# Kernel optimization log

Measured on AMD Instinct MI355X. Metric: run time of the kernel, lower is better.

The kernel has to match this reference:

```python
import jax, jax.numpy as jnp
import numpy as np

L1, L2, B = 512, 512, 2
D1, D2, BN = 256, 256, 256
NEG = jnp.float32(-1e12)


def setup_inputs() -> dict:
    key = jax.random.key(0)
    ks = jax.random.split(key, 8)
    s = 0.05
    return {
        "ctx_1": jax.random.normal(ks[0], (L1, B, D1), jnp.float32),
        "ctx_2": jax.random.normal(ks[1], (L2, B, D2), jnp.float32),
        "ctx_1_mask": jnp.ones((L1, B), jnp.float32),
        "ctx_2_mask": jnp.ones((L2, B), jnp.float32),
        # mlp_hid: Conv2d(D1+D2 -> BN, 1x1) with bias
        "Wh": jax.random.normal(ks[2], (D1 + D2, BN), jnp.float32) * s,
        "bh": jnp.zeros((BN,), jnp.float32),
        # mlp_out: Conv2d(BN -> 1, 1x1), bias=False (mlp_bias default)
        "wo": jax.random.normal(ks[3], (BN,), jnp.float32) * s,
        # project_1_to_2 / project_2_to_1: Linear(D1+D2 -> BN) with bias
        "W12": jax.random.normal(ks[4], (D2 + D1, BN), jnp.float32) * s,
        "b12": jnp.zeros((BN,), jnp.float32),
        "W21": jax.random.normal(ks[5], (D1 + D2, BN), jnp.float32) * s,
        "b21": jnp.zeros((BN,), jnp.float32),
    }


def reference(ctx_1, ctx_2, ctx_1_mask, ctx_2_mask, Wh, bh, wo, W12, b12, W21, b21):
    d1 = ctx_1.shape[-1]
    # 1x1 conv on cat([b_ctx_1, b_ctx_2]) == sum of two independent projections
    Wh1, Wh2 = Wh[:d1], Wh[d1:]
    p1 = jnp.einsum('lbd,dk->blk', ctx_1, Wh1)            # (B, L1, K)
    p2 = jnp.einsum('mbd,dk->bmk', ctx_2, Wh2)            # (B, L2, K)
    hidden = jnp.tanh(p1[:, :, None, :] + p2[:, None, :, :] + bh)  # (B, L1, L2, K)
    affinity = jnp.einsum('blmk,k->blm', hidden, wo)      # (B, L1, L2)
    # masked in both directions
    affinity = affinity + (1.0 - ctx_1_mask.T)[:, :, None] * NEG
    affinity = affinity + (1.0 - ctx_2_mask.T)[:, None, :] * NEG
    # 1 -> 2 direction: softmax over L2
    dist_1_to_2 = jax.nn.softmax(affinity, axis=2)        # (B, L1, L2)
    context_1_to_2 = jnp.einsum('lbd,blm->mbd', ctx_1, dist_1_to_2)  # (L2, B, D1)
    seq_1_to_2 = jnp.tanh(jnp.concatenate([ctx_2, context_1_to_2], axis=-1) @ W12 + b12)
    # 2 -> 1 direction: softmax over L1 (then contracted over L2, as in the torch code)
    dist_2_to_1 = jax.nn.softmax(affinity, axis=1)        # (B, L1, L2)
    context_2_to_1 = jnp.einsum('mbd,blm->lbd', ctx_2, dist_2_to_1)  # (L1, B, D2)
    seq_2_to_1 = jnp.tanh(jnp.concatenate([ctx_1, context_2_to_1], axis=-1) @ W21 + b21)
    return (seq_2_to_1, seq_1_to_2)
```

## Files before the change

### kernel.cpp

```cpp
#include <hip/hip_runtime.h>


#define NEGC (-1e12f)
#define TWO_LOG2E 2.8853900817779268f
#define LOG2E 1.4426950408889634f
#define N2LOG2E (-2.8853900817779268f)

typedef __attribute__((ext_vector_type(8))) short bf16x8;
typedef __attribute__((ext_vector_type(4))) float f32x4;

__device__ __forceinline__ short f2bf(float x)
{
    union { float f; unsigned u; } v; v.f = x;
    unsigned r = (v.u + 0x7FFFu + ((v.u >> 16) & 1u)) >> 16;
    return (short)r;
}

__global__ __launch_bounds__(256) void k_proj(
    const float* __restrict__ ctx1, const float* __restrict__ ctx2,
    const float* __restrict__ Wh, const float* __restrict__ bh,
    const float* __restrict__ W12, const float* __restrict__ b12,
    const float* __restrict__ W21, const float* __restrict__ b21,
    const float* __restrict__ mask1, const float* __restrict__ mask2,
    float* __restrict__ E1, float* __restrict__ E2,
    float* __restrict__ P12, float* __restrict__ U1,
    float* __restrict__ P21, float* __restrict__ U2,
    float* __restrict__ p1, float* __restrict__ p2,
    float* __restrict__ S1, float* __restrict__ S2)
{
    const int t  = threadIdx.x;
    const int g  = blockIdx.z;
    const int r0 = blockIdx.x * 64;
    const int n0 = blockIdx.y * 64;

    const float* A; const float* W; const float* bias; int expm; float* outp;
    switch (g) {
      case 0:  A=ctx1; W=Wh;        bias=bh;   expm=1; outp=E1;  break;
      case 1:  A=ctx2; W=Wh+65536;  bias=0;    expm=1; outp=E2;  break;
      case 2:  A=ctx2; W=W12;       bias=b12;  expm=0; outp=P12; break;
      case 3:  A=ctx1; W=W12+65536; bias=0;    expm=0; outp=U1;  break;
      case 4:  A=ctx1; W=W21;       bias=b21;  expm=0; outp=P21; break;
      default: A=ctx2; W=W21+65536; bias=0;    expm=0; outp=U2;  break;
    }

    if (g == 0 && blockIdx.x == 0 && blockIdx.y == 0) {
        for (int idx = t; idx < 1024; idx += 256) {
            int row = idx >> 1, b = idx & 1;
            p1[b * 512 + row] = __builtin_amdgcn_exp2f(LOG2E * (1.f - mask1[idx]) * NEGC);
            p2[b * 512 + row] = __builtin_amdgcn_exp2f(LOG2E * (1.f - mask2[idx]) * NEGC);
            S1[b * 512 + row] = 0.f;
            S2[b * 512 + row] = 0.f;
        }
    }

    __shared__ __align__(16) short Abf[64 * 136];
    __shared__ __align__(16) short Bbf[64 * 136];

    const int w    = t >> 6;
    const int lane = t & 63;
    const int quad = lane >> 4;
    const int lr   = lane & 15;

    f32x4 acc[4] = {};

    for (int kc = 0; kc < 256; kc += 128) {
        #pragma unroll
        for (int i = 0; i < 8; ++i) {
            int slot = i * 256 + t;
            int r = slot >> 5, kq = (slot & 31) << 2;
            float4 v = *(const float4*)(A + (r0 + r) * 256 + kc + kq);
            short4 s; s.x = f2bf(v.x); s.y = f2bf(v.y); s.z = f2bf(v.z); s.w = f2bf(v.w);
            *(short4*)(Abf + r * 136 + kq) = s;
        }
        #pragma unroll
        for (int i = 0; i < 8; ++i) {
            int slot = i * 256 + t;
            int bk = slot >> 4, bn4 = (slot & 15) << 2;
            float4 v = *(const float4*)(W + (kc + bk) * 256 + n0 + bn4);
            Bbf[(bn4 + 0) * 136 + bk] = f2bf(v.x);
            Bbf[(bn4 + 1) * 136 + bk] = f2bf(v.y);
            Bbf[(bn4 + 2) * 136 + bk] = f2bf(v.z);
            Bbf[(bn4 + 3) * 136 + bk] = f2bf(v.w);
        }
        __syncthreads();
        #pragma unroll
        for (int s = 0; s < 4; ++s) {
            const int kb = s * 32 + quad * 8;
            bf16x8 a = *(const bf16x8*)(Abf + (w * 16 + lr) * 136 + kb);
            #pragma unroll
            for (int nc = 0; nc < 4; ++nc) {
                bf16x8 b = *(const bf16x8*)(Bbf + (nc * 16 + lr) * 136 + kb);
                acc[nc] = __builtin_amdgcn_mfma_f32_16x16x32_bf16(a, b, acc[nc], 0, 0, 0);
            }
        }
        __syncthreads();
    }

    #pragma unroll
    for (int nc = 0; nc < 4; ++nc) {
        const int col = n0 + nc * 16 + lr;
        const float bv = bias ? bias[col] : 0.f;
        #pragma unroll
        for (int reg = 0; reg < 4; ++reg) {
            int row  = r0 + w * 16 + quad * 4 + reg;
            int orow = ((row & 1) << 9) + (row >> 1);
            float v = acc[nc][reg] + bv;
            if (expm) v = __builtin_amdgcn_exp2f(v * TWO_LOG2E);
            outp[orow * 256 + col] = v;
        }
    }
}

#define PAIR(AV, QV, WV, ACC) do {                                    \
    float x0_ = fmaf(AV.x, QV.x, 1.f);                                \
    float x1_ = fmaf(AV.y, QV.y, 1.f);                                \
    float x2_ = fmaf(AV.z, QV.z, 1.f);                                \
    float x3_ = fmaf(AV.w, QV.w, 1.f);                                \
    float r01_ = __builtin_amdgcn_rcpf(x0_ * x1_);                    \
    float r23_ = __builtin_amdgcn_rcpf(x2_ * x3_);                    \
    float z01_ = fmaf(WV.y, x0_, WV.x * x1_);                         \
    float z23_ = fmaf(WV.w, x2_, WV.z * x3_);                         \
    ACC = fmaf(r01_, z01_, ACC);                                      \
    ACC = fmaf(r23_, z23_, ACC);                                      \
} while (0)

__global__ __launch_bounds__(256) void k_aff(
    const float* __restrict__ E1g, const float* __restrict__ E2g,
    const float* __restrict__ wo,
    const float* __restrict__ p1g, const float* __restrict__ p2g,
    float* __restrict__ EN, float* __restrict__ ET,
    float* __restrict__ S1, float* __restrict__ S2)
{
    const int t  = threadIdx.x;
    const int l0 = blockIdx.x * 32, m0 = blockIdx.y * 32, b = blockIdx.z;

    __shared__ __align__(16) float E1s[32 * 132];
    __shared__ __align__(16) float E2s[32 * 132];
    __shared__ __align__(16) float affs[32 * 36];

    const int tl = t >> 4, tm = t & 15;
    float acc[2][2] = {};

    for (int kc = 0; kc < 256; kc += 128) {
        #pragma unroll
        for (int i = 0; i < 4; ++i) {
            int slot = i * 256 + t;
            int r = slot >> 5, kq = (slot & 31) << 2;
            *(float4*)(E1s + r * 132 + kq) =
                *(const float4*)(E1g + (((b << 9) + l0 + r) << 8) + kc + kq);
            *(float4*)(E2s + r * 132 + kq) =
                *(const float4*)(E2g + (((b << 9) + m0 + r) << 8) + kc + kq);
        }
        __syncthreads();
        #pragma unroll 4
        for (int k0 = 0; k0 < 128; k0 += 4) {
            const float4 w  = *(const float4*)(wo + kc + k0);
            const float4 a0 = *(const float4*)(E1s + tl * 132 + k0);
            const float4 a1 = *(const float4*)(E1s + (tl + 16) * 132 + k0);
            const float4 q0 = *(const float4*)(E2s + tm * 132 + k0);
            const float4 q1 = *(const float4*)(E2s + (tm + 16) * 132 + k0);
            PAIR(a0, q0, w, acc[0][0]);
            PAIR(a0, q1, w, acc[0][1]);
            PAIR(a1, q0, w, acc[1][0]);
            PAIR(a1, q1, w, acc[1][1]);
        }
        __syncthreads();
    }

    affs[tl * 36 + tm]             = __builtin_amdgcn_exp2f(acc[0][0] * N2LOG2E);
    affs[tl * 36 + tm + 16]        = __builtin_amdgcn_exp2f(acc[0][1] * N2LOG2E);
    affs[(tl + 16) * 36 + tm]      = __builtin_amdgcn_exp2f(acc[1][0] * N2LOG2E);
    affs[(tl + 16) * 36 + tm + 16] = __builtin_amdgcn_exp2f(acc[1][1] * N2LOG2E);
    __syncthreads();

    const int r  = t >> 3;
    const int c4 = (t & 7) << 2;
    {
        float4 e = *(const float4*)(affs + r * 36 + c4);
        const float p1r = p1g[(b << 9) + l0 + r];
        float4 vn = make_float4(e.x * p1r, e.y * p1r, e.z * p1r, e.w * p1r);
        *(float4*)(EN + (((b << 9) + l0 + r) << 9) + m0 + c4) = vn;
        float4 p2v = *(const float4*)(p2g + (b << 9) + m0 + c4);
        float s = (e.x * p2v.x + e.y * p2v.y) + (e.z * p2v.z + e.w * p2v.w);
        s += __shfl_xor(s, 1, 64);
        s += __shfl_xor(s, 2, 64);
        s += __shfl_xor(s, 4, 64);
        if ((t & 7) == 0) atomicAdd(S1 + (b << 9) + l0 + r, s);
    }
    {
        float4 te;
        te.x = affs[(c4 + 0) * 36 + r];
        te.y = affs[(c4 + 1) * 36 + r];
        te.z = affs[(c4 + 2) * 36 + r];
        te.w = affs[(c4 + 3) * 36 + r];
        const float p2r = p2g[(b << 9) + m0 + r];
        float4 vt = make_float4(te.x * p2r, te.y * p2r, te.z * p2r, te.w * p2r);
        *(float4*)(ET + (((b << 9) + m0 + r) << 9) + l0 + c4) = vt;
        float4 p1v = *(const float4*)(p1g + (b << 9) + l0 + c4);
        float s = (te.x * p1v.x + te.y * p1v.y) + (te.z * p1v.z + te.w * p1v.w);
        s += __shfl_xor(s, 1, 64);
        s += __shfl_xor(s, 2, 64);
        s += __shfl_xor(s, 4, 64);
        if ((t & 7) == 0) atomicAdd(S2 + (b << 9) + m0 + r, s);
    }
}

__global__ __launch_bounds__(256) void k_final(
    const float* __restrict__ EN, const float* __restrict__ ET,
    const float* __restrict__ U1, const float* __restrict__ U2,
    const float* __restrict__ P12, const float* __restrict__ P21,
    const float* __restrict__ S1, const float* __restrict__ S2,
    float* __restrict__ out)
{
    const int t   = threadIdx.x;
    const int r0  = blockIdx.x * 32, n0 = blockIdx.y * 32;
    const int dir = blockIdx.z >> 1, b = blockIdx.z & 1;
    const float* Ag = (dir == 0 ? ET  : EN)  + b * 262144;
    const float* Sg = (dir == 0 ? S1  : S2)  + b * 512;
    const float* Bg = (dir == 0 ? U1  : U2)  + b * 131072;
    const float* Pg = (dir == 0 ? P12 : P21) + b * 131072;
    float* o = out + (dir == 0 ? 262144 : 0);

    __shared__ __align__(16) short Abf[32 * 72];
    __shared__ __align__(16) short Bbf[32 * 72];
    __shared__ __align__(16) float rs[512];

    for (int i = t; i < 512; i += 256)
        rs[i] = __builtin_amdgcn_rcpf(Sg[i]);
    __syncthreads();

    const int w    = t >> 6;
    const int lane = t & 63;
    const int quad = lane >> 4;
    const int lr   = lane & 15;
    const int wr   = (w >> 1) << 4, wc = (w & 1) << 4;
    f32x4 acc = {};

    for (int kc = 0; kc < 512; kc += 64) {
        #pragma unroll
        for (int i = 0; i < 2; ++i) {
            int slot = i * 256 + t;
            int r = slot >> 4, kq = (slot & 15) << 2;
            float4 v = *(const float4*)(Ag + ((r0 + r) << 9) + kc + kq);
            const float* rp = rs + kc + kq;
            short4 s;
            s.x = f2bf(v.x * rp[0]); s.y = f2bf(v.y * rp[1]);
            s.z = f2bf(v.z * rp[2]); s.w = f2bf(v.w * rp[3]);
            *(short4*)(Abf + r * 72 + kq) = s;
        }
        #pragma unroll
        for (int i = 0; i < 2; ++i) {
            int slot = i * 256 + t;
            int bk = slot >> 3, bn4 = (slot & 7) << 2;
            float4 v = *(const float4*)(Bg + ((kc + bk) << 8) + n0 + bn4);
            Bbf[(bn4 + 0) * 72 + bk] = f2bf(v.x);
            Bbf[(bn4 + 1) * 72 + bk] = f2bf(v.y);
            Bbf[(bn4 + 2) * 72 + bk] = f2bf(v.z);
            Bbf[(bn4 + 3) * 72 + bk] = f2bf(v.w);
        }
        __syncthreads();
        #pragma unroll
        for (int s = 0; s < 2; ++s) {
            const int kb = s * 32 + quad * 8;
            bf16x8 a = *(const bf16x8*)(Abf + (wr + lr) * 72 + kb);
            bf16x8 bb = *(const bf16x8*)(Bbf + (wc + lr) * 72 + kb);
            acc = __builtin_amdgcn_mfma_f32_16x16x32_bf16(a, bb, acc, 0, 0, 0);
        }
        __syncthreads();
    }

    const int col = n0 + wc + lr;
    #pragma unroll
    for (int reg = 0; reg < 4; ++reg) {
        const int m = r0 + wr + quad * 4 + reg;
        float v = acc[reg] + Pg[(m << 8) + col];
        float tv = 1.f - 2.f * __builtin_amdgcn_rcpf(
                       __builtin_amdgcn_exp2f(v * TWO_LOG2E) + 1.f);
        o[((m << 1) + b) * 256 + col] = tv;
    }
}

extern "C" void kernel_launch(void* const* d_in, const int* in_sizes, int n_in,
                              void* d_out, int out_size, void* d_ws, size_t ws_size,
                              hipStream_t stream)
{
    const float* ctx1 = (const float*)d_in[0];
    const float* ctx2 = (const float*)d_in[1];
    const float* m1   = (const float*)d_in[2];
    const float* m2   = (const float*)d_in[3];
    const float* Wh   = (const float*)d_in[4];
    const float* bh   = (const float*)d_in[5];
    const float* wo   = (const float*)d_in[6];
    const float* W12  = (const float*)d_in[7];
    const float* b12  = (const float*)d_in[8];
    const float* W21  = (const float*)d_in[9];
    const float* b21  = (const float*)d_in[10];
    float* out = (float*)d_out;
    float* ws  = (float*)d_ws;

    float* E1  = ws;
    float* E2  = E1  + 262144;
    float* P12 = E2  + 262144;
    float* U1  = P12 + 262144;
    float* P21 = U1  + 262144;
    float* U2  = P21 + 262144;
    float* p1  = U2  + 262144;
    float* p2  = p1  + 1024;
    float* S1  = p2  + 1024;
    float* S2  = S1  + 1024;
    float* EN  = S2  + 1024;
    float* ET  = EN  + 524288;

    hipLaunchKernelGGL(k_proj, dim3(16, 4, 6), dim3(256), 0, stream,
                       ctx1, ctx2, Wh, bh, W12, b12, W21, b21, m1, m2,
                       E1, E2, P12, U1, P21, U2, p1, p2, S1, S2);
    hipLaunchKernelGGL(k_aff, dim3(16, 16, 2), dim3(256), 0, stream,
                       E1, E2, wo, p1, p2, EN, ET, S1, S2);
    hipLaunchKernelGGL(k_final, dim3(16, 8, 4), dim3(256), 0, stream,
                       EN, ET, U1, U2, P12, P21, S1, S2, out);
}
```

Measured before the change: 118.4 us.

## Overlap output-projection GEMMs with affinity kernel via interleaved block roles

The first kernel now computes only the two Wh projections (E1/E2). The four output-side projections (P12, U1, P21, U2) move into a combined middle kernel. Every third block runs an MFMA GEMM tile and the other blocks compute affinity tiles, so the independent GEMMs share the machine with the affinity pass instead of sitting on the critical path of the first kernel. The cost is a larger shared-memory footprint per block, since the union buffer is sized for the bigger role, and possible load imbalance between heterogeneous blocks.

```diff
diff --git a/kernel.cpp b/kernel.cpp
--- a/kernel.cpp
+++ b/kernel.cpp
@@ -16,15 +16,11 @@
     return (short)r;
 }
 
-__global__ __launch_bounds__(256) void k_proj(
+__global__ __launch_bounds__(256) void k_projE(
     const float* __restrict__ ctx1, const float* __restrict__ ctx2,
     const float* __restrict__ Wh, const float* __restrict__ bh,
-    const float* __restrict__ W12, const float* __restrict__ b12,
-    const float* __restrict__ W21, const float* __restrict__ b21,
     const float* __restrict__ mask1, const float* __restrict__ mask2,
     float* __restrict__ E1, float* __restrict__ E2,
-    float* __restrict__ P12, float* __restrict__ U1,
-    float* __restrict__ P21, float* __restrict__ U2,
     float* __restrict__ p1, float* __restrict__ p2,
     float* __restrict__ S1, float* __restrict__ S2)
 {
@@ -33,15 +29,10 @@
     const int r0 = blockIdx.x * 64;
     const int n0 = blockIdx.y * 64;
 
-    const float* A; const float* W; const float* bias; int expm; float* outp;
-    switch (g) {
-      case 0:  A=ctx1; W=Wh;        bias=bh;   expm=1; outp=E1;  break;
-      case 1:  A=ctx2; W=Wh+65536;  bias=0;    expm=1; outp=E2;  break;
-      case 2:  A=ctx2; W=W12;       bias=b12;  expm=0; outp=P12; break;
-      case 3:  A=ctx1; W=W12+65536; bias=0;    expm=0; outp=U1;  break;
-      case 4:  A=ctx1; W=W21;       bias=b21;  expm=0; outp=P21; break;
-      default: A=ctx2; W=W21+65536; bias=0;    expm=0; outp=U2;  break;
-    }
+    const float* A    = g ? ctx2       : ctx1;
+    const float* W    = g ? Wh + 65536 : Wh;
+    const float* bias = g ? 0          : bh;
+    float*       outp = g ? E2         : E1;
 
     if (g == 0 && blockIdx.x == 0 && blockIdx.y == 0) {
         for (int idx = t; idx < 1024; idx += 256) {
@@ -105,8 +96,7 @@
             int row  = r0 + w * 16 + quad * 4 + reg;
             int orow = ((row & 1) << 9) + (row >> 1);
             float v = acc[nc][reg] + bv;
-            if (expm) v = __builtin_amdgcn_exp2f(v * TWO_LOG2E);
-            outp[orow * 256 + col] = v;
+            outp[orow * 256 + col] = __builtin_amdgcn_exp2f(v * TWO_LOG2E);
         }
     }
 }
@@ -124,84 +114,167 @@
     ACC = fmaf(r23_, z23_, ACC);                                      \
 } while (0)
 
-__global__ __launch_bounds__(256) void k_aff(
+__global__ __launch_bounds__(256) void k_mid(
+    const float* __restrict__ ctx1, const float* __restrict__ ctx2,
+    const float* __restrict__ W12, const float* __restrict__ b12,
+    const float* __restrict__ W21, const float* __restrict__ b21,
     const float* __restrict__ E1g, const float* __restrict__ E2g,
     const float* __restrict__ wo,
     const float* __restrict__ p1g, const float* __restrict__ p2g,
+    float* __restrict__ P12, float* __restrict__ U1,
+    float* __restrict__ P21, float* __restrict__ U2,
     float* __restrict__ EN, float* __restrict__ ET,
     float* __restrict__ S1, float* __restrict__ S2)
 {
-    const int t  = threadIdx.x;
-    const int l0 = blockIdx.x * 32, m0 = blockIdx.y * 32, b = blockIdx.z;
-
-    __shared__ __align__(16) float E1s[32 * 132];
-    __shared__ __align__(16) float E2s[32 * 132];
-    __shared__ __align__(16) float affs[32 * 36];
-
-    const int tl = t >> 4, tm = t & 15;
-    float acc[2][2] = {};
-
-    for (int kc = 0; kc < 256; kc += 128) {
-        #pragma unroll
-        for (int i = 0; i < 4; ++i) {
-            int slot = i * 256 + t;
-            int r = slot >> 5, kq = (slot & 31) << 2;
-            *(float4*)(E1s + r * 132 + kq) =
-                *(const float4*)(E1g + (((b << 9) + l0 + r) << 8) + kc + kq);
-            *(float4*)(E2s + r * 132 + kq) =
-                *(const float4*)(E2g + (((b << 9) + m0 + r) << 8) + kc + kq);
-        }
-        __syncthreads();
-        #pragma unroll 4
-        for (int k0 = 0; k0 < 128; k0 += 4) {
-            const float4 w  = *(const float4*)(wo + kc + k0);
-            const float4 a0 = *(const float4*)(E1s + tl * 132 + k0);
-            const float4 a1 = *(const float4*)(E1s + (tl + 16) * 132 + k0);
-            const float4 q0 = *(const float4*)(E2s + tm * 132 + k0);
-            const float4 q1 = *(const float4*)(E2s + (tm + 16) * 132 + k0);
-            PAIR(a0, q0, w, acc[0][0]);
-            PAIR(a0, q1, w, acc[0][1]);
-            PAIR(a1, q0, w, acc[1][0]);
-            PAIR(a1, q1, w, acc[1][1]);
-        }
-        __syncthreads();
-    }
-
-    affs[tl * 36 + tm]             = __builtin_amdgcn_exp2f(acc[0][0] * N2LOG2E);
-    affs[tl * 36 + tm + 16]        = __builtin_amdgcn_exp2f(acc[0][1] * N2LOG2E);
-    affs[(tl + 16) * 36 + tm]      = __builtin_amdgcn_exp2f(acc[1][0] * N2LOG2E);
-    affs[(tl + 16) * 36 + tm + 16] = __builtin_amdgcn_exp2f(acc[1][1] * N2LOG2E);
-    __syncthreads();
-
-    const int r  = t >> 3;
-    const int c4 = (t & 7) << 2;
-    {
-        float4 e = *(const float4*)(affs + r * 36 + c4);
-        const float p1r = p1g[(b << 9) + l0 + r];
-        float4 vn = make_float4(e.x * p1r, e.y * p1r, e.z * p1r, e.w * p1r);
-        *(float4*)(EN + (((b << 9) + l0 + r) << 9) + m0 + c4) = vn;
-        float4 p2v = *(const float4*)(p2g + (b << 9) + m0 + c4);
-        float s = (e.x * p2v.x + e.y * p2v.y) + (e.z * p2v.z + e.w * p2v.w);
-        s += __shfl_xor(s, 1, 64);
-        s += __shfl_xor(s, 2, 64);
-        s += __shfl_xor(s, 4, 64);
-        if ((t & 7) == 0) atomicAdd(S1 + (b << 9) + l0 + r, s);
-    }
-    {
-        float4 te;
-        te.x = affs[(c4 + 0) * 36 + r];
-        te.y = affs[(c4 + 1) * 36 + r];
-        te.z = affs[(c4 + 2) * 36 + r];
-        te.w = affs[(c4 + 3) * 36 + r];
-        const float p2r = p2g[(b << 9) + m0 + r];
-        float4 vt = make_float4(te.x * p2r, te.y * p2r, te.z * p2r, te.w * p2r);
-        *(float4*)(ET + (((b << 9) + m0 + r) << 9) + l0 + c4) = vt;
-        float4 p1v = *(const float4*)(p1g + (b << 9) + l0 + c4);
-        float s = (te.x * p1v.x + te.y * p1v.y) + (te.z * p1v.z + te.w * p1v.w);
-        s += __shfl_xor(s, 1, 64);
-        s += __shfl_xor(s, 2, 64);
-        s += __shfl_xor(s, 4, 64);
-        if ((t & 7) == 0) atomicAdd(S2 + (b << 9) + m0 + r, s);
+    __shared__ __align__(16) char smem[38400];
+
+    const int t   = threadIdx.x;
+    const int bid = blockIdx.x;
+    const int r3  = bid % 3;
+
+    if (r3 == 2) {
+        const int idx = bid / 3;
+        const int g   = idx >> 6;
+        const int r0  = (idx & 15) * 64;
+        const int n0  = ((idx >> 4) & 3) * 64;
+
+        const float* A; const float* W; const float* bias; float* outp;
+        switch (g) {
+          case 0:  A = ctx2; W = W12;         bias = b12; outp = P12; break;
+          case 1:  A = ctx1; W = W12 + 65536; bias = 0;   outp = U1;  break;
+          case 2:  A = ctx1; W = W21;         bias = b21; outp = P21; break;
+          default: A = ctx2; W = W21 + 65536; bias = 0;   outp = U2;  break;
+        }
+
+        short* Abf = (short*)smem;
+        short* Bbf = Abf + 64 * 136;
+
+        const int w    = t >> 6;
+        const int lane = t & 63;
+        const int quad = lane >> 4;
+        const int lr   = lane & 15;
+
+        f32x4 acc[4] = {};
+
+        for (int kc = 0; kc < 256; kc += 128) {
+            #pragma unroll
+            for (int i = 0; i < 8; ++i) {
+                int slot = i * 256 + t;
+                int r = slot >> 5, kq = (slot & 31) << 2;
+                float4 v = *(const float4*)(A + (r0 + r) * 256 + kc + kq);
+                short4 s; s.x = f2bf(v.x); s.y = f2bf(v.y); s.z = f2bf(v.z); s.w = f2bf(v.w);
+                *(short4*)(Abf + r * 136 + kq) = s;
+            }
+            #pragma unroll
+            for (int i = 0; i < 8; ++i) {
+                int slot = i * 256 + t;
+                int bk = slot >> 4, bn4 = (slot & 15) << 2;
+                float4 v = *(const float4*)(W + (kc + bk) * 256 + n0 + bn4);
+                Bbf[(bn4 + 0) * 136 + bk] = f2bf(v.x);
+                Bbf[(bn4 + 1) * 136 + bk] = f2bf(v.y);
+                Bbf[(bn4 + 2) * 136 + bk] = f2bf(v.z);
+                Bbf[(bn4 + 3) * 136 + bk] = f2bf(v.w);
+            }
+            __syncthreads();
+            #pragma unroll
+            for (int s = 0; s < 4; ++s) {
+                const int kb = s * 32 + quad * 8;
+                bf16x8 a = *(const bf16x8*)(Abf + (w * 16 + lr) * 136 + kb);
+                #pragma unroll
+                for (int nc = 0; nc < 4; ++nc) {
+                    bf16x8 b = *(const bf16x8*)(Bbf + (nc * 16 + lr) * 136 + kb);
+                    acc[nc] = __builtin_amdgcn_mfma_f32_16x16x32_bf16(a, b, acc[nc], 0, 0, 0);
+                }
+            }
+            __syncthreads();
+        }
+
+        #pragma unroll
+        for (int nc = 0; nc < 4; ++nc) {
+            const int col = n0 + nc * 16 + lr;
+            const float bv = bias ? bias[col] : 0.f;
+            #pragma unroll
+            for (int reg = 0; reg < 4; ++reg) {
+                int row  = r0 + w * 16 + quad * 4 + reg;
+                int orow = ((row & 1) << 9) + (row >> 1);
+                outp[orow * 256 + col] = acc[nc][reg] + bv;
+            }
+        }
+    } else {
+        const int aidx = (bid / 3) * 2 + r3;
+        const int l0 = (aidx & 15) * 32;
+        const int m0 = ((aidx >> 4) & 15) * 32;
+        const int b  = aidx >> 8;
+
+        float* E1s  = (float*)smem;
+        float* E2s  = E1s + 32 * 132;
+        float* affs = E2s + 32 * 132;
+
+        const int tl = t >> 4, tm = t & 15;
+        float acc[2][2] = {};
+
+        for (int kc = 0; kc < 256; kc += 128) {
+            #pragma unroll
+            for (int i = 0; i < 4; ++i) {
+                int slot = i * 256 + t;
+                int r = slot >> 5, kq = (slot & 31) << 2;
+                *(float4*)(E1s + r * 132 + kq) =
+                    *(const float4*)(E1g + (((b << 9) + l0 + r) << 8) + kc + kq);
+                *(float4*)(E2s + r * 132 + kq) =
+                    *(const float4*)(E2g + (((b << 9) + m0 + r) << 8) + kc + kq);
+            }
+            __syncthreads();
+            #pragma unroll 4
+            for (int k0 = 0; k0 < 128; k0 += 4) {
+                const float4 w  = *(const float4*)(wo + kc + k0);
+                const float4 a0 = *(const float4*)(E1s + tl * 132 + k0);
+                const float4 a1 = *(const float4*)(E1s + (tl + 16) * 132 + k0);
+                const float4 q0 = *(const float4*)(E2s + tm * 132 + k0);
+                const float4 q1 = *(const float4*)(E2s + (tm + 16) * 132 + k0);
+                PAIR(a0, q0, w, acc[0][0]);
+                PAIR(a0, q1, w, acc[0][1]);
+                PAIR(a1, q0, w, acc[1][0]);
+                PAIR(a1, q1, w, acc[1][1]);
+            }
+            __syncthreads();
+        }
+
+        affs[tl * 36 + tm]             = __builtin_amdgcn_exp2f(acc[0][0] * N2LOG2E);
+        affs[tl * 36 + tm + 16]        = __builtin_amdgcn_exp2f(acc[0][1] * N2LOG2E);
+        affs[(tl + 16) * 36 + tm]      = __builtin_amdgcn_exp2f(acc[1][0] * N2LOG2E);
+        affs[(tl + 16) * 36 + tm + 16] = __builtin_amdgcn_exp2f(acc[1][1] * N2LOG2E);
+        __syncthreads();
+
+        const int r  = t >> 3;
+        const int c4 = (t & 7) << 2;
+        {
+            float4 e = *(const float4*)(affs + r * 36 + c4);
+            const float p1r = p1g[(b << 9) + l0 + r];
+            float4 vn = make_float4(e.x * p1r, e.y * p1r, e.z * p1r, e.w * p1r);
+            *(float4*)(EN + (((b << 9) + l0 + r) << 9) + m0 + c4) = vn;
+            float4 p2v = *(const float4*)(p2g + (b << 9) + m0 + c4);
+            float s = (e.x * p2v.x + e.y * p2v.y) + (e.z * p2v.z + e.w * p2v.w);
+            s += __shfl_xor(s, 1, 64);
+            s += __shfl_xor(s, 2, 64);
+            s += __shfl_xor(s, 4, 64);
+            if ((t & 7) == 0) atomicAdd(S1 + (b << 9) + l0 + r, s);
+        }
+        {
+            float4 te;
+            te.x = affs[(c4 + 0) * 36 + r];
+            te.y = affs[(c4 + 1) * 36 + r];
+            te.z = affs[(c4 + 2) * 36 + r];
+            te.w = affs[(c4 + 3) * 36 + r];
+            const float p2r = p2g[(b << 9) + m0 + r];
+            float4 vt = make_float4(te.x * p2r, te.y * p2r, te.z * p2r, te.w * p2r);
+            *(float4*)(ET + (((b << 9) + m0 + r) << 9) + l0 + c4) = vt;
+            float4 p1v = *(const float4*)(p1g + (b << 9) + l0 + c4);
+            float s = (te.x * p1v.x + te.y * p1v.y) + (te.z * p1v.z + te.w * p1v.w);
+            s += __shfl_xor(s, 1, 64);
+            s += __shfl_xor(s, 2, 64);
+            s += __shfl_xor(s, 4, 64);
+            if ((t & 7) == 0) atomicAdd(S2 + (b << 9) + m0 + r, s);
+        }
     }
 }
 
@@ -311,11 +384,12 @@
     float* EN  = S2  + 1024;
     float* ET  = EN  + 524288;
 
-    hipLaunchKernelGGL(k_proj, dim3(16, 4, 6), dim3(256), 0, stream,
-                       ctx1, ctx2, Wh, bh, W12, b12, W21, b21, m1, m2,
-                       E1, E2, P12, U1, P21, U2, p1, p2, S1, S2);
-    hipLaunchKernelGGL(k_aff, dim3(16, 16, 2), dim3(256), 0, stream,
-                       E1, E2, wo, p1, p2, EN, ET, S1, S2);
+    hipLaunchKernelGGL(k_projE, dim3(16, 4, 2), dim3(256), 0, stream,
+                       ctx1, ctx2, Wh, bh, m1, m2, E1, E2, p1, p2, S1, S2);
+    hipLaunchKernelGGL(k_mid, dim3(768, 1, 1), dim3(256), 0, stream,
+                       ctx1, ctx2, W12, b12, W21, b21,
+                       E1, E2, wo, p1, p2,
+                       P12, U1, P21, U2, EN, ET, S1, S2);
     hipLaunchKernelGGL(k_final, dim3(16, 8, 4), dim3(256), 0, stream,
                        EN, ET, U1, U2, P12, P21, S1, S2, out);
 }
```

Measured after the change: 116.8 us. About the same (-1.4%).

## Fuse three kernels into one cooperative persistent kernel with grid syncs

Applied to the files above, without the earlier changes.

Merges the projection, affinity and final GEMM kernels into a single cooperative launch of 512 blocks, separated by grid-wide barriers, with stages sharing a reused shared-memory buffer. This removes two kernel launch boundaries and their gaps. The final stage also uses a K chunk of 128 instead of 64, halving its loop iterations and barriers. In exchange, all blocks must be co-resident (launch bounds of 2 per SM), grid.sync adds its own cost, and the projection stage leaves 128 blocks idle.

```diff
diff --git a/kernel.cpp b/kernel.cpp
--- a/kernel.cpp
+++ b/kernel.cpp
@@ -1,4 +1,7 @@
 #include <hip/hip_runtime.h>
+#include <hip/hip_cooperative_groups.h>
+
+namespace cg = cooperative_groups;
 
 
 #define NEGC (-1e12f)
@@ -14,101 +17,6 @@
     union { float f; unsigned u; } v; v.f = x;
     unsigned r = (v.u + 0x7FFFu + ((v.u >> 16) & 1u)) >> 16;
     return (short)r;
-}
-
-__global__ __launch_bounds__(256) void k_proj(
-    const float* __restrict__ ctx1, const float* __restrict__ ctx2,
-    const float* __restrict__ Wh, const float* __restrict__ bh,
-    const float* __restrict__ W12, const float* __restrict__ b12,
-    const float* __restrict__ W21, const float* __restrict__ b21,
-    const float* __restrict__ mask1, const float* __restrict__ mask2,
-    float* __restrict__ E1, float* __restrict__ E2,
-    float* __restrict__ P12, float* __restrict__ U1,
-    float* __restrict__ P21, float* __restrict__ U2,
-    float* __restrict__ p1, float* __restrict__ p2,
-    float* __restrict__ S1, float* __restrict__ S2)
-{
-    const int t  = threadIdx.x;
-    const int g  = blockIdx.z;
-    const int r0 = blockIdx.x * 64;
-    const int n0 = blockIdx.y * 64;
-
-    const float* A; const float* W; const float* bias; int expm; float* outp;
-    switch (g) {
-      case 0:  A=ctx1; W=Wh;        bias=bh;   expm=1; outp=E1;  break;
-      case 1:  A=ctx2; W=Wh+65536;  bias=0;    expm=1; outp=E2;  break;
-      case 2:  A=ctx2; W=W12;       bias=b12;  expm=0; outp=P12; break;
-      case 3:  A=ctx1; W=W12+65536; bias=0;    expm=0; outp=U1;  break;
-      case 4:  A=ctx1; W=W21;       bias=b21;  expm=0; outp=P21; break;
-      default: A=ctx2; W=W21+65536; bias=0;    expm=0; outp=U2;  break;
-    }
-
-    if (g == 0 && blockIdx.x == 0 && blockIdx.y == 0) {
-        for (int idx = t; idx < 1024; idx += 256) {
-            int row = idx >> 1, b = idx & 1;
-            p1[b * 512 + row] = __builtin_amdgcn_exp2f(LOG2E * (1.f - mask1[idx]) * NEGC);
-            p2[b * 512 + row] = __builtin_amdgcn_exp2f(LOG2E * (1.f - mask2[idx]) * NEGC);
-            S1[b * 512 + row] = 0.f;
-            S2[b * 512 + row] = 0.f;
-        }
-    }
-
-    __shared__ __align__(16) short Abf[64 * 136];
-    __shared__ __align__(16) short Bbf[64 * 136];
-
-    const int w    = t >> 6;
-    const int lane = t & 63;
-    const int quad = lane >> 4;
-    const int lr   = lane & 15;
-
-    f32x4 acc[4] = {};
-
-    for (int kc = 0; kc < 256; kc += 128) {
-        #pragma unroll
-        for (int i = 0; i < 8; ++i) {
-            int slot = i * 256 + t;
-            int r = slot >> 5, kq = (slot & 31) << 2;
-            float4 v = *(const float4*)(A + (r0 + r) * 256 + kc + kq);
-            short4 s; s.x = f2bf(v.x); s.y = f2bf(v.y); s.z = f2bf(v.z); s.w = f2bf(v.w);
-            *(short4*)(Abf + r * 136 + kq) = s;
-        }
-        #pragma unroll
-        for (int i = 0; i < 8; ++i) {
-            int slot = i * 256 + t;
-            int bk = slot >> 4, bn4 = (slot & 15) << 2;
-            float4 v = *(const float4*)(W + (kc + bk) * 256 + n0 + bn4);
-            Bbf[(bn4 + 0) * 136 + bk] = f2bf(v.x);
-            Bbf[(bn4 + 1) * 136 + bk] = f2bf(v.y);
-            Bbf[(bn4 + 2) * 136 + bk] = f2bf(v.z);
-            Bbf[(bn4 + 3) * 136 + bk] = f2bf(v.w);
-        }
-        __syncthreads();
-        #pragma unroll
-        for (int s = 0; s < 4; ++s) {
-            const int kb = s * 32 + quad * 8;
-            bf16x8 a = *(const bf16x8*)(Abf + (w * 16 + lr) * 136 + kb);
-            #pragma unroll
-            for (int nc = 0; nc < 4; ++nc) {
-                bf16x8 b = *(const bf16x8*)(Bbf + (nc * 16 + lr) * 136 + kb);
-                acc[nc] = __builtin_amdgcn_mfma_f32_16x16x32_bf16(a, b, acc[nc], 0, 0, 0);
-            }
-        }
-        __syncthreads();
-    }
-
-    #pragma unroll
-    for (int nc = 0; nc < 4; ++nc) {
-        const int col = n0 + nc * 16 + lr;
-        const float bv = bias ? bias[col] : 0.f;
-        #pragma unroll
-        for (int reg = 0; reg < 4; ++reg) {
-            int row  = r0 + w * 16 + quad * 4 + reg;
-            int orow = ((row & 1) << 9) + (row >> 1);
-            float v = acc[nc][reg] + bv;
-            if (expm) v = __builtin_amdgcn_exp2f(v * TWO_LOG2E);
-            outp[orow * 256 + col] = v;
-        }
-    }
 }
 
 #define PAIR(AV, QV, WV, ACC) do {                                    \
@@ -124,159 +32,272 @@
     ACC = fmaf(r23_, z23_, ACC);                                      \
 } while (0)
 
-__global__ __launch_bounds__(256) void k_aff(
-    const float* __restrict__ E1g, const float* __restrict__ E2g,
+__global__ __launch_bounds__(256, 2) void k_fused(
+    const float* __restrict__ ctx1, const float* __restrict__ ctx2,
+    const float* __restrict__ mask1, const float* __restrict__ mask2,
+    const float* __restrict__ Wh, const float* __restrict__ bh,
     const float* __restrict__ wo,
-    const float* __restrict__ p1g, const float* __restrict__ p2g,
-    float* __restrict__ EN, float* __restrict__ ET,
-    float* __restrict__ S1, float* __restrict__ S2)
+    const float* __restrict__ W12, const float* __restrict__ b12,
+    const float* __restrict__ W21, const float* __restrict__ b21,
+    float* __restrict__ ws, float* __restrict__ out)
 {
-    const int t  = threadIdx.x;
-    const int l0 = blockIdx.x * 32, m0 = blockIdx.y * 32, b = blockIdx.z;
-
-    __shared__ __align__(16) float E1s[32 * 132];
-    __shared__ __align__(16) float E2s[32 * 132];
-    __shared__ __align__(16) float affs[32 * 36];
-
-    const int tl = t >> 4, tm = t & 15;
-    float acc[2][2] = {};
-
-    for (int kc = 0; kc < 256; kc += 128) {
+    float* E1  = ws;
+    float* E2  = E1  + 262144;
+    float* P12 = E2  + 262144;
+    float* U1  = P12 + 262144;
+    float* P21 = U1  + 262144;
+    float* U2  = P21 + 262144;
+    float* p1  = U2  + 262144;
+    float* p2  = p1  + 1024;
+    float* S1  = p2  + 1024;
+    float* S2  = S1  + 1024;
+    float* EN  = S2  + 1024;
+    float* ET  = EN  + 524288;
+
+    __shared__ __align__(16) char smem[38400];
+
+    const int t   = threadIdx.x;
+    const int bid = blockIdx.x;
+
+    if (bid == 0) {
+        for (int idx = t; idx < 1024; idx += 256) {
+            int row = idx >> 1, b = idx & 1;
+            p1[b * 512 + row] = __builtin_amdgcn_exp2f(LOG2E * (1.f - mask1[idx]) * NEGC);
+            p2[b * 512 + row] = __builtin_amdgcn_exp2f(LOG2E * (1.f - mask2[idx]) * NEGC);
+            S1[b * 512 + row] = 0.f;
+            S2[b * 512 + row] = 0.f;
+        }
+    }
+
+    if (bid < 384) {
+        const float* A; const float* W; const float* bias; float* outp; int expm;
+        int r0, n0;
+        if (bid < 128) {
+            const int g = bid >> 6, i6 = bid & 63;
+            r0 = (i6 & 15) * 64; n0 = (i6 >> 4) * 64;
+            A = g ? ctx2 : ctx1; W = g ? Wh + 65536 : Wh;
+            bias = g ? 0 : bh; outp = g ? E2 : E1; expm = 1;
+        } else {
+            const int idx = bid - 128;
+            const int g = idx >> 6;
+            r0 = (idx & 15) * 64; n0 = ((idx >> 4) & 3) * 64;
+            expm = 0;
+            switch (g) {
+              case 0:  A = ctx2; W = W12;         bias = b12; outp = P12; break;
+              case 1:  A = ctx1; W = W12 + 65536; bias = 0;   outp = U1;  break;
+              case 2:  A = ctx1; W = W21;         bias = b21; outp = P21; break;
+              default: A = ctx2; W = W21 + 65536; bias = 0;   outp = U2;  break;
+            }
+        }
+
+        short* Abf = (short*)smem;
+        short* Bbf = Abf + 64 * 136;
+
+        const int w    = t >> 6;
+        const int lane = t & 63;
+        const int quad = lane >> 4;
+        const int lr   = lane & 15;
+
+        f32x4 acc[4] = {};
+
+        for (int kc = 0; kc < 256; kc += 128) {
+            #pragma unroll
+            for (int i = 0; i < 8; ++i) {
+                int slot = i * 256 + t;
+                int r = slot >> 5, kq = (slot & 31) << 2;
+                float4 v = *(const float4*)(A + (r0 + r) * 256 + kc + kq);
+                short4 s; s.x = f2bf(v.x); s.y = f2bf(v.y); s.z = f2bf(v.z); s.w = f2bf(v.w);
+                *(short4*)(Abf + r * 136 + kq) = s;
+            }
+            #pragma unroll
+            for (int i = 0; i < 8; ++i) {
+                int slot = i * 256 + t;
+                int bk = slot >> 4, bn4 = (slot & 15) << 2;
+                float4 v = *(const float4*)(W + (kc + bk) * 256 + n0 + bn4);
+                Bbf[(bn4 + 0) * 136 + bk] = f2bf(v.x);
+                Bbf[(bn4 + 1) * 136 + bk] = f2bf(v.y);
+                Bbf[(bn4 + 2) * 136 + bk] = f2bf(v.z);
+                Bbf[(bn4 + 3) * 136 + bk] = f2bf(v.w);
+            }
+            __syncthreads();
+            #pragma unroll
+            for (int s = 0; s < 4; ++s) {
+                const int kb = s * 32 + quad * 8;
+                bf16x8 a = *(const bf16x8*)(Abf + (w * 16 + lr) * 136 + kb);
+                #pragma unroll
+                for (int nc = 0; nc < 4; ++nc) {
+                    bf16x8 b = *(const bf16x8*)(Bbf + (nc * 16 + lr) * 136 + kb);
+                    acc[nc] = __builtin_amdgcn_mfma_f32_16x16x32_bf16(a, b, acc[nc], 0, 0, 0);
+                }
+            }
+            __syncthreads();
+        }
+
         #pragma unroll
-        for (int i = 0; i < 4; ++i) {
-            int slot = i * 256 + t;
-            int r = slot >> 5, kq = (slot & 31) << 2;
-            *(float4*)(E1s + r * 132 + kq) =
-                *(const float4*)(E1g + (((b << 9) + l0 + r) << 8) + kc + kq);
-            *(float4*)(E2s + r * 132 + kq) =
-                *(const float4*)(E2g + (((b << 9) + m0 + r) << 8) + kc + kq);
-        }
+        for (int nc = 0; nc < 4; ++nc) {
+            const int col = n0 + nc * 16 + lr;
+            const float bv = bias ? bias[col] : 0.f;
+            #pragma unroll
+            for (int reg = 0; reg < 4; ++reg) {
+                int row  = r0 + w * 16 + quad * 4 + reg;
+                int orow = ((row & 1) << 9) + (row >> 1);
+                float v = acc[nc][reg] + bv;
+                if (expm) v = __builtin_amdgcn_exp2f(v * TWO_LOG2E);
+                outp[orow * 256 + col] = v;
+            }
+        }
+    }
+
+    __threadfence();
+    cg::this_grid().sync();
+
+    {
+        const int l0 = (bid & 15) * 32;
+        const int m0 = ((bid >> 4) & 15) * 32;
+        const int b  = bid >> 8;
+
+        float* E1s  = (float*)smem;
+        float* E2s  = E1s + 32 * 132;
+        float* affs = E2s + 32 * 132;
+
+        const int tl = t >> 4, tm = t & 15;
+        float acc[2][2] = {};
+
+        for (int kc = 0; kc < 256; kc += 128) {
+            #pragma unroll
+            for (int i = 0; i < 4; ++i) {
+                int slot = i * 256 + t;
+                int r = slot >> 5, kq = (slot & 31) << 2;
+                *(float4*)(E1s + r * 132 + kq) =
+                    *(const float4*)(E1 + (((b << 9) + l0 + r) << 8) + kc + kq);
+                *(float4*)(E2s + r * 132 + kq) =
+                    *(const float4*)(E2 + (((b << 9) + m0 + r) << 8) + kc + kq);
+            }
+            __syncthreads();
+            #pragma unroll 4
+            for (int k0 = 0; k0 < 128; k0 += 4) {
+                const float4 w  = *(const float4*)(wo + kc + k0);
+                const float4 a0 = *(const float4*)(E1s + tl * 132 + k0);
+                const float4 a1 = *(const float4*)(E1s + (tl + 16) * 132 + k0);
+                const float4 q0 = *(const float4*)(E2s + tm * 132 + k0);
+                const float4 q1 = *(const float4*)(E2s + (tm + 16) * 132 + k0);
+                PAIR(a0, q0, w, acc[0][0]);
+                PAIR(a0, q1, w, acc[0][1]);
+                PAIR(a1, q0, w, acc[1][0]);
+                PAIR(a1, q1, w, acc[1][1]);
+            }
+            __syncthreads();
+        }
+
+        affs[tl * 36 + tm]             = __builtin_amdgcn_exp2f(acc[0][0] * N2LOG2E);
+        affs[tl * 36 + tm + 16]        = __builtin_amdgcn_exp2f(acc[0][1] * N2LOG2E);
+        affs[(tl + 16) * 36 + tm]      = __builtin_amdgcn_exp2f(acc[1][0] * N2LOG2E);
+        affs[(tl + 16) * 36 + tm + 16] = __builtin_amdgcn_exp2f(acc[1][1] * N2LOG2E);
         __syncthreads();
-        #pragma unroll 4
-        for (int k0 = 0; k0 < 128; k0 += 4) {
-            const float4 w  = *(const float4*)(wo + kc + k0);
-            const float4 a0 = *(const float4*)(E1s + tl * 132 + k0);
-            const float4 a1 = *(const float4*)(E1s + (tl + 16) * 132 + k0);
-            const float4 q0 = *(const float4*)(E2s + tm * 132 + k0);
-            const float4 q1 = *(const float4*)(E2s + (tm + 16) * 132 + k0);
-            PAIR(a0, q0, w, acc[0][0]);
-            PAIR(a0, q1, w, acc[0][1]);
-            PAIR(a1, q0, w, acc[1][0]);
-            PAIR(a1, q1, w, acc[1][1]);
-        }
+
+        const int r  = t >> 3;
+        const int c4 = (t & 7) << 2;
+        {
+            float4 e = *(const float4*)(affs + r * 36 + c4);
+            const float p1r = p1[(b << 9) + l0 + r];
+            float4 vn = make_float4(e.x * p1r, e.y * p1r, e.z * p1r, e.w * p1r);
+            *(float4*)(EN + (((b << 9) + l0 + r) << 9) + m0 + c4) = vn;
+            float4 p2v = *(const float4*)(p2 + (b << 9) + m0 + c4);
+            float s = (e.x * p2v.x + e.y * p2v.y) + (e.z * p2v.z + e.w * p2v.w);
+            s += __shfl_xor(s, 1, 64);
+            s += __shfl_xor(s, 2, 64);
+            s += __shfl_xor(s, 4, 64);
+            if ((t & 7) == 0) atomicAdd(S1 + (b << 9) + l0 + r, s);
+        }
+        {
+            float4 te;
+            te.x = affs[(c4 + 0) * 36 + r];
+            te.y = affs[(c4 + 1) * 36 + r];
+            te.z = affs[(c4 + 2) * 36 + r];
+            te.w = affs[(c4 + 3) * 36 + r];
+            const float p2r = p2[(b << 9) + m0 + r];
+            float4 vt = make_float4(te.x * p2r, te.y * p2r, te.z * p2r, te.w * p2r);
+            *(float4*)(ET + (((b << 9) + m0 + r) << 9) + l0 + c4) = vt;
+            float4 p1v = *(const float4*)(p1 + (b << 9) + l0 + c4);
+            float s = (te.x * p1v.x + te.y * p1v.y) + (te.z * p1v.z + te.w * p1v.w);
+            s += __shfl_xor(s, 1, 64);
+            s += __shfl_xor(s, 2, 64);
+            s += __shfl_xor(s, 4, 64);
+            if ((t & 7) == 0) atomicAdd(S2 + (b << 9) + m0 + r, s);
+        }
+    }
+
+    __threadfence();
+    cg::this_grid().sync();
+
+    {
+        const int r0  = (bid & 15) * 32;
+        const int n0  = ((bid >> 4) & 7) * 32;
+        const int z   = bid >> 7;
+        const int dir = z >> 1, b = z & 1;
+        const float* Ag = (dir == 0 ? ET  : EN)  + b * 262144;
+        const float* Sg = (dir == 0 ? S1  : S2)  + b * 512;
+        const float* Bg = (dir == 0 ? U1  : U2)  + b * 131072;
+        const float* Pg = (dir == 0 ? P12 : P21) + b * 131072;
+        float* o = out + (dir == 0 ? 262144 : 0);
+
+        short* Abf = (short*)smem;
+        short* Bbf = Abf + 32 * 136;
+        float* rs  = (float*)(Bbf + 32 * 136);
+
+        for (int i = t; i < 512; i += 256)
+            rs[i] = __builtin_amdgcn_rcpf(Sg[i]);
         __syncthreads();
-    }
-
-    affs[tl * 36 + tm]             = __builtin_amdgcn_exp2f(acc[0][0] * N2LOG2E);
-    affs[tl * 36 + tm + 16]        = __builtin_amdgcn_exp2f(acc[0][1] * N2LOG2E);
-    affs[(tl + 16) * 36 + tm]      = __builtin_amdgcn_exp2f(acc[1][0] * N2LOG2E);
-    affs[(tl + 16) * 36 + tm + 16] = __builtin_amdgcn_exp2f(acc[1][1] * N2LOG2E);
-    __syncthreads();
-
-    const int r  = t >> 3;
-    const int c4 = (t & 7) << 2;
-    {
-        float4 e = *(const float4*)(affs + r * 36 + c4);
-        const float p1r = p1g[(b << 9) + l0 + r];
-        float4 vn = make_float4(e.x * p1r, e.y * p1r, e.z * p1r, e.w * p1r);
-        *(float4*)(EN + (((b << 9) + l0 + r) << 9) + m0 + c4) = vn;
-        float4 p2v = *(const float4*)(p2g + (b << 9) + m0 + c4);
-        float s = (e.x * p2v.x + e.y * p2v.y) + (e.z * p2v.z + e.w * p2v.w);
-        s += __shfl_xor(s, 1, 64);
-        s += __shfl_xor(s, 2, 64);
-        s += __shfl_xor(s, 4, 64);
-        if ((t & 7) == 0) atomicAdd(S1 + (b << 9) + l0 + r, s);
-    }
-    {
-        float4 te;
-        te.x = affs[(c4 + 0) * 36 + r];
-        te.y = affs[(c4 + 1) * 36 + r];
-        te.z = affs[(c4 + 2) * 36 + r];
-        te.w = affs[(c4 + 3) * 36 + r];
-        const float p2r = p2g[(b << 9) + m0 + r];
-        float4 vt = make_float4(te.x * p2r, te.y * p2r, te.z * p2r, te.w * p2r);
-        *(float4*)(ET + (((b << 9) + m0 + r) << 9) + l0 + c4) = vt;
-        float4 p1v = *(const float4*)(p1g + (b << 9) + l0 + c4);
-        float s = (te.x * p1v.x + te.y * p1v.y) + (te.z * p1v.z + te.w * p1v.w);
-        s += __shfl_xor(s, 1, 64);
-        s += __shfl_xor(s, 2, 64);
-        s += __shfl_xor(s, 4, 64);
-        if ((t & 7) == 0) atomicAdd(S2 + (b << 9) + m0 + r, s);
-    }
-}
-
-__global__ __launch_bounds__(256) void k_final(
-    const float* __restrict__ EN, const float* __restrict__ ET,
-    const float* __restrict__ U1, const float* __restrict__ U2,
-    const float* __restrict__ P12, const float* __restrict__ P21,
-    const float* __restrict__ S1, const float* __restrict__ S2,
-    float* __restrict__ out)
-{
-    const int t   = threadIdx.x;
-    const int r0  = blockIdx.x * 32, n0 = blockIdx.y * 32;
-    const int dir = blockIdx.z >> 1, b = blockIdx.z & 1;
-    const float* Ag = (dir == 0 ? ET  : EN)  + b * 262144;
-    const float* Sg = (dir == 0 ? S1  : S2)  + b * 512;
-    const float* Bg = (dir == 0 ? U1  : U2)  + b * 131072;
-    const float* Pg = (dir == 0 ? P12 : P21) + b * 131072;
-    float* o = out + (dir == 0 ? 262144 : 0);
-
-    __shared__ __align__(16) short Abf[32 * 72];
-    __shared__ __align__(16) short Bbf[32 * 72];
-    __shared__ __align__(16) float rs[512];
-
-    for (int i = t; i < 512; i += 256)
-        rs[i] = __builtin_amdgcn_rcpf(Sg[i]);
-    __syncthreads();
-
-    const int w    = t >> 6;
-    const int lane = t & 63;
-    const int quad = lane >> 4;
-    const int lr   = lane & 15;
-    const int wr   = (w >> 1) << 4, wc = (w & 1) << 4;
-    f32x4 acc = {};
-
-    for (int kc = 0; kc < 512; kc += 64) {
+
+        const int w    = t >> 6;
+        const int lane = t & 63;
+        const int quad = lane >> 4;
+        const int lr   = lane & 15;
+        const int wr   = (w >> 1) << 4, wc = (w & 1) << 4;
+        f32x4 acc = {};
+
+        for (int kc = 0; kc < 512; kc += 128) {
+            #pragma unroll
+            for (int i = 0; i < 4; ++i) {
+                int slot = i * 256 + t;
+                int r = slot >> 5, kq = (slot & 31) << 2;
+                float4 v = *(const float4*)(Ag + ((r0 + r) << 9) + kc + kq);
+                const float* rp = rs + kc + kq;
+                short4 s;
+                s.x = f2bf(v.x * rp[0]); s.y = f2bf(v.y * rp[1]);
+                s.z = f2bf(v.z * rp[2]); s.w = f2bf(v.w * rp[3]);
+                *(short4*)(Abf + r * 136 + kq) = s;
+            }
+            #pragma unroll
+            for (int i = 0; i < 4; ++i) {
+                int slot = i * 256 + t;
+                int bk = slot >> 3, bn4 = (slot & 7) << 2;
+                float4 v = *(const float4*)(Bg + ((kc + bk) << 8) + n0 + bn4);
+                Bbf[(bn4 + 0) * 136 + bk] = f2bf(v.x);
+                Bbf[(bn4 + 1) * 136 + bk] = f2bf(v.y);
+                Bbf[(bn4 + 2) * 136 + bk] = f2bf(v.z);
+                Bbf[(bn4 + 3) * 136 + bk] = f2bf(v.w);
+            }
+            __syncthreads();
+            #pragma unroll
+            for (int s = 0; s < 4; ++s) {
+                const int kb = s * 32 + quad * 8;
+                bf16x8 a  = *(const bf16x8*)(Abf + (wr + lr) * 136 + kb);
+                bf16x8 bb = *(const bf16x8*)(Bbf + (wc + lr) * 136 + kb);
+                acc = __builtin_amdgcn_mfma_f32_16x16x32_bf16(a, bb, acc, 0, 0, 0);
+            }
+            __syncthreads();
+        }
+
+        const int col = n0 + wc + lr;
         #pragma unroll
-        for (int i = 0; i < 2; ++i) {
-            int slot = i * 256 + t;
-            int r = slot >> 4, kq = (slot & 15) << 2;
-            float4 v = *(const float4*)(Ag + ((r0 + r) << 9) + kc + kq);
-            const float* rp = rs + kc + kq;
-            short4 s;
-            s.x = f2bf(v.x * rp[0]); s.y = f2bf(v.y * rp[1]);
-            s.z = f2bf(v.z * rp[2]); s.w = f2bf(v.w * rp[3]);
-            *(short4*)(Abf + r * 72 + kq) = s;
-        }
-        #pragma unroll
-        for (int i = 0; i < 2; ++i) {
-            int slot = i * 256 + t;
-            int bk = slot >> 3, bn4 = (slot & 7) << 2;
-            float4 v = *(const float4*)(Bg + ((kc + bk) << 8) + n0 + bn4);
-            Bbf[(bn4 + 0) * 72 + bk] = f2bf(v.x);
-            Bbf[(bn4 + 1) * 72 + bk] = f2bf(v.y);
-            Bbf[(bn4 + 2) * 72 + bk] = f2bf(v.z);
-            Bbf[(bn4 + 3) * 72 + bk] = f2bf(v.w);
-        }
-        __syncthreads();
-        #pragma unroll
-        for (int s = 0; s < 2; ++s) {
-            const int kb = s * 32 + quad * 8;
-            bf16x8 a = *(const bf16x8*)(Abf + (wr + lr) * 72 + kb);
-            bf16x8 bb = *(const bf16x8*)(Bbf + (wc + lr) * 72 + kb);
-            acc = __builtin_amdgcn_mfma_f32_16x16x32_bf16(a, bb, acc, 0, 0, 0);
-        }
-        __syncthreads();
-    }
-
-    const int col = n0 + wc + lr;
-    #pragma unroll
-    for (int reg = 0; reg < 4; ++reg) {
-        const int m = r0 + wr + quad * 4 + reg;
-        float v = acc[reg] + Pg[(m << 8) + col];
-        float tv = 1.f - 2.f * __builtin_amdgcn_rcpf(
-                       __builtin_amdgcn_exp2f(v * TWO_LOG2E) + 1.f);
-        o[((m << 1) + b) * 256 + col] = tv;
+        for (int reg = 0; reg < 4; ++reg) {
+            const int m = r0 + wr + quad * 4 + reg;
+            float v = acc[reg] + Pg[(m << 8) + col];
+            float tv = 1.f - 2.f * __builtin_amdgcn_rcpf(
+                           __builtin_amdgcn_exp2f(v * TWO_LOG2E) + 1.f);
+            o[((m << 1) + b) * 256 + col] = tv;
+        }
     }
 }
 
@@ -298,24 +319,10 @@
     float* out = (float*)d_out;
     float* ws  = (float*)d_ws;
 
-    float* E1  = ws;
-    float* E2  = E1  + 262144;
-    float* P12 = E2  + 262144;
-    float* U1  = P12 + 262144;
-    float* P21 = U1  + 262144;
-    float* U2  = P21 + 262144;
-    float* p1  = U2  + 262144;
-    float* p2  = p1  + 1024;
-    float* S1  = p2  + 1024;
-    float* S2  = S1  + 1024;
-    float* EN  = S2  + 1024;
-    float* ET  = EN  + 524288;
-
-    hipLaunchKernelGGL(k_proj, dim3(16, 4, 6), dim3(256), 0, stream,
-                       ctx1, ctx2, Wh, bh, W12, b12, W21, b21, m1, m2,
-                       E1, E2, P12, U1, P21, U2, p1, p2, S1, S2);
-    hipLaunchKernelGGL(k_aff, dim3(16, 16, 2), dim3(256), 0, stream,
-                       E1, E2, wo, p1, p2, EN, ET, S1, S2);
-    hipLaunchKernelGGL(k_final, dim3(16, 8, 4), dim3(256), 0, stream,
-                       EN, ET, U1, U2, P12, P21, S1, S2, out);
+    void* args[] = { (void*)&ctx1, (void*)&ctx2, (void*)&m1, (void*)&m2,
+                     (void*)&Wh, (void*)&bh, (void*)&wo,
+                     (void*)&W12, (void*)&b12, (void*)&W21, (void*)&b21,
+                     (void*)&ws, (void*)&out };
+    hipLaunchCooperativeKernel((const void*)k_fused, dim3(512), dim3(256),
+                               args, 0, stream);
 }
```

Measured after the change: 336.6 us. 184% more time.
